# Kernel tuning notes

Hardware: AMD Instinct MI355X
Metric: run time of the kernel (lower is better)

The kernel has to match this reference:

```python
import jax, jax.numpy as jnp
import numpy as np

H = 1024
NH = 16
DH = H // NH

def setup_inputs() -> dict:
    key = jax.random.key(0)
    ks = jax.random.split(key, 6)
    s = 1.0 / np.sqrt(H)
    x = jax.random.normal(ks[0], (4, 2048, H), dtype=jnp.float32)
    Wq = jax.random.uniform(ks[1], (H, H), jnp.float32, -s, s)
    Wk = jax.random.uniform(ks[2], (H, H), jnp.float32, -s, s)
    Wv = jax.random.uniform(ks[3], (H, H), jnp.float32, -s, s)
    Wo = jax.random.uniform(ks[4], (H, H), jnp.float32, -s, s)
    bo = jax.random.uniform(ks[5], (H,), jnp.float32, -s, s)
    return {"x": x, "Wq": Wq, "Wk": Wk, "Wv": Wv, "Wo": Wo, "bo": bo}

def reference(x, Wq, Wk, Wv, Wo, bo):
    B, T, Hd = x.shape
    # projections: torch Linear is x @ W.T
    def split_heads(y):
        return y.reshape(B, T, NH, DH).transpose(0, 2, 1, 3)  # [B, nh, T, dh]
    Q = split_heads(x @ Wq.T)
    K = split_heads(x @ Wk.T)
    V = split_heads(x @ Wv.T)
    scores = jnp.einsum('bhtd,bhsd->bhts', Q, K) / jnp.sqrt(jnp.float32(DH))
    w = jax.nn.softmax(scores, axis=-1)
    ctx = jnp.einsum('bhts,bhsd->bhtd', w, V)  # [B, nh, T, dh]
    ctx = ctx.transpose(0, 2, 1, 3).reshape(B, T, Hd)
    out = ctx @ Wo.T + bo  # [B, T, H]
    return out.mean(axis=1)  # [B, H]
```

## Files before the change

kernel.cpp:

```cpp
#include <hip/hip_runtime.h>
#include <hip/hip_bf16.h>
#include <cstdint>

#define BB   4
#define TT   2048
#define HH   1024
#define NHH  16
#define DHH  64
#define MM   (BB*TT)
#define N3   (3*HH)

typedef __attribute__((ext_vector_type(8))) short short8;
typedef __attribute__((ext_vector_type(4))) float f32x4;

#if __has_builtin(__builtin_amdgcn_exp2f)
#define EXP2F(x) __builtin_amdgcn_exp2f(x)
#else
#define EXP2F(x) exp2f(x)
#endif

#define QSCALE 0.1803368801111204f

__device__ __forceinline__ float bf2f(unsigned short u) {
    return __uint_as_float(((uint32_t)u) << 16);
}
__device__ __forceinline__ unsigned short f2bf(float f) {
    uint32_t u = __float_as_uint(f);
    return (unsigned short)((u + 0x7fffu + ((u >> 16) & 1u)) >> 16);
}
__device__ __forceinline__ void gload_lds16(const unsigned short* g, unsigned short* l) {
    __builtin_amdgcn_global_load_lds(
        (const __attribute__((address_space(1))) uint32_t*)g,
        (__attribute__((address_space(3))) uint32_t*)l, 16, 0, 0);
}

__global__ __launch_bounds__(256) void cvt_bf16(
    const float* __restrict__ src, unsigned short* __restrict__ dst, int n4)
{
    int i = blockIdx.x * 256 + threadIdx.x;
    const int stride = gridDim.x * 256;
    for (; i < n4; i += stride) {
        float4 v = ((const float4*)src)[i];
        ushort4 o;
        o.x = f2bf(v.x); o.y = f2bf(v.y); o.z = f2bf(v.z); o.w = f2bf(v.w);
        ((ushort4*)dst)[i] = o;
    }
}

__global__ __launch_bounds__(256) void cvt_w3(
    const float* __restrict__ Wq, const float* __restrict__ Wk,
    const float* __restrict__ Wv, unsigned short* __restrict__ Wb)
{
    const float* src = (blockIdx.y == 0) ? Wq : (blockIdx.y == 1 ? Wk : Wv);
    unsigned short* dst = Wb + (size_t)blockIdx.y * HH * HH;
    const int n4 = HH * HH / 4;
    int i = blockIdx.x * 256 + threadIdx.x;
    const int stride = gridDim.x * 256;
    for (; i < n4; i += stride) {
        float4 v = ((const float4*)src)[i];
        ushort4 o;
        o.x = f2bf(v.x); o.y = f2bf(v.y); o.z = f2bf(v.z); o.w = f2bf(v.w);
        ((ushort4*)dst)[i] = o;
    }
}

__global__ __launch_bounds__(256) void proj_mfma(
    const unsigned short* __restrict__ xb, const unsigned short* __restrict__ Wb,
    unsigned short* __restrict__ qp, unsigned short* __restrict__ kp,
    unsigned short* __restrict__ vp)
{
    __shared__ unsigned short As[4096];
    __shared__ unsigned short Bs[4096];
    const int m0 = blockIdx.x * 128;
    const int n0 = blockIdx.y * 128;
    const int sel = n0 >> 10;
    const unsigned short* Wbase = Wb + (size_t)sel * HH * HH;
    const int nw0 = n0 & (HH - 1);
    const int tid = threadIdx.x;
    const int wave = tid >> 6, lane = tid & 63;
    const int quad = lane >> 4, l15 = lane & 15;
    const int wm = wave >> 1, wn = wave & 1;

    f32x4 acc[4][4];
    #pragma unroll
    for (int i = 0; i < 4; ++i)
        #pragma unroll
        for (int j = 0; j < 4; ++j) acc[i][j] = (f32x4){0.f, 0.f, 0.f, 0.f};

    for (int k0 = 0; k0 < HH; k0 += 32) {
        __syncthreads();
        #pragma unroll
        for (int q = 0; q < 2; ++q) {
            const int chunk = (wave * 2 + q) * 64 + lane;
            const int kc = chunk >> 7, mrow = chunk & 127;
            gload_lds16(xb    + (size_t)(m0  + mrow) * HH + k0 + kc * 8, As + chunk * 8);
            gload_lds16(Wbase + (size_t)(nw0 + mrow) * HH + k0 + kc * 8, Bs + chunk * 8);
        }
        __syncthreads();
        short8 af[4], bf[4];
        #pragma unroll
        for (int i = 0; i < 4; ++i)
            af[i] = *(const short8*)&As[(quad * 128 + wm * 64 + i * 16 + l15) * 8];
        #pragma unroll
        for (int j = 0; j < 4; ++j)
            bf[j] = *(const short8*)&Bs[(quad * 128 + wn * 64 + j * 16 + l15) * 8];
        #pragma unroll
        for (int i = 0; i < 4; ++i)
            #pragma unroll
            for (int j = 0; j < 4; ++j)
                acc[i][j] = __builtin_amdgcn_mfma_f32_16x16x32_bf16(af[i], bf[j], acc[i][j], 0, 0, 0);
    }

    unsigned short* outp = (sel == 0) ? qp : (sel == 1 ? kp : vp);
    const float cscale = (sel == 0) ? QSCALE : 1.0f;

    unsigned short* eb = As;
    const int lr_st = tid >> 3;
    const int k8    = tid & 7;
    const int row_g = m0 + ((lr_st & 16) ? 64 : 0) + (lr_st & 15);
    #pragma unroll
    for (int i = 0; i < 4; ++i) {
        __syncthreads();
        #pragma unroll
        for (int j = 0; j < 4; ++j) {
            const int c = wn * 64 + j * 16 + l15;
            #pragma unroll
            for (int r = 0; r < 4; ++r)
                eb[(wm * 16 + quad * 4 + r) * 128 + c] = f2bf(acc[i][j][r] * cscale);
        }
        __syncthreads();
        const int row = row_g + i * 16;
        const int bb2 = row >> 11, tt2 = row & (TT - 1);
        {
            const int col = n0 + k8 * 8;
            const int hh2 = (col >> 6) & (NHH - 1);
            *(short8*)(&outp[((size_t)(bb2 * NHH + hh2) * TT + tt2) * DHH + (col & 63)]) =
                *(const short8*)(&eb[lr_st * 128 + k8 * 8]);
        }
        {
            const int col = n0 + 64 + k8 * 8;
            const int hh2 = (col >> 6) & (NHH - 1);
            *(short8*)(&outp[((size_t)(bb2 * NHH + hh2) * TT + tt2) * DHH + (col & 63)]) =
                *(const short8*)(&eb[lr_st * 128 + 64 + k8 * 8]);
        }
    }
}

__global__ __launch_bounds__(256) void attn_fused(
    const unsigned short* __restrict__ qp, const unsigned short* __restrict__ kp,
    float* __restrict__ a)
{
    const int h = blockIdx.x, b = blockIdx.z;
    const int t0 = blockIdx.y * 128;
    const int bh = b * NHH + h;
    const int tid = threadIdx.x;
    const int wave = tid >> 6, lane = tid & 63;
    const int quad = lane >> 4, l15 = lane & 15;
    __shared__ float red[4][128];
    __shared__ float linv[128];

    const unsigned short* q = qp + (size_t)bh * TT * DHH;
    const unsigned short* kbase =
        kp + (size_t)bh * TT * DHH + (size_t)(wave * 512 + l15) * DHH + quad * 8;

    short8 aq[8][2];
    #pragma unroll
    for (int i = 0; i < 8; ++i)
        #pragma unroll
        for (int c = 0; c < 2; ++c)
            aq[i][c] = *(const short8*)&q[(size_t)(t0 + i * 16 + l15) * DHH + quad * 8 + c * 32];

    const f32x4 zk = {0.f, 0.f, 0.f, 0.f};

    float rs[8][4];
    #pragma unroll
    for (int i = 0; i < 8; ++i)
        #pragma unroll
        for (int r = 0; r < 4; ++r) rs[i][r] = 0.f;

    {
        const unsigned short* kw = kbase;
        short8 c0a = *(const short8*)(kw);
        short8 c0b = *(const short8*)(kw + 32);
        kw += 16 * DHH;
        short8 c1a = *(const short8*)(kw);
        short8 c1b = *(const short8*)(kw + 32);
        kw += 16 * DHH;
        for (int ss = 0; ss < 32; ++ss) {
            const short8 ba = c0a, bb = c0b;
            c0a = c1a; c0b = c1b;
            if (ss < 30) {
                c1a = *(const short8*)(kw);
                c1b = *(const short8*)(kw + 32);
            }
            kw += 16 * DHH;
            f32x4 pc = __builtin_amdgcn_mfma_f32_16x16x32_bf16(aq[0][0], ba, zk, 0, 0, 0);
            pc = __builtin_amdgcn_mfma_f32_16x16x32_bf16(aq[0][1], bb, pc, 0, 0, 0);
            #pragma unroll
            for (int i = 1; i < 8; ++i) {
                f32x4 c = __builtin_amdgcn_mfma_f32_16x16x32_bf16(aq[i][0], ba, zk, 0, 0, 0);
                c = __builtin_amdgcn_mfma_f32_16x16x32_bf16(aq[i][1], bb, c, 0, 0, 0);
                #pragma unroll
                for (int r = 0; r < 4; ++r) rs[i - 1][r] += EXP2F(pc[r]);
                pc = c;
            }
            #pragma unroll
            for (int r = 0; r < 4; ++r) rs[7][r] += EXP2F(pc[r]);
        }
    }
    #pragma unroll
    for (int off = 1; off < 16; off <<= 1)
        #pragma unroll
        for (int i = 0; i < 8; ++i)
            #pragma unroll
            for (int r = 0; r < 4; ++r) rs[i][r] += __shfl_xor(rs[i][r], off);
    if (l15 == 0)
        #pragma unroll
        for (int i = 0; i < 8; ++i)
            #pragma unroll
            for (int r = 0; r < 4; ++r) red[wave][i * 16 + quad * 4 + r] = rs[i][r];
    __syncthreads();
    if (tid < 128) {
        const float l = red[0][tid] + red[1][tid] + red[2][tid] + red[3][tid];
        linv[tid] = 1.0f / (l * (float)TT);
    }
    __syncthreads();

    float lrv[8][4];
    #pragma unroll
    for (int i = 0; i < 8; ++i)
        #pragma unroll
        for (int r = 0; r < 4; ++r) lrv[i][r] = linv[i * 16 + quad * 4 + r];

    float* ap = a + (size_t)bh * TT + wave * 512 + l15;

    {
        const unsigned short* kw = kbase;
        short8 c0a = *(const short8*)(kw);
        short8 c0b = *(const short8*)(kw + 32);
        kw += 16 * DHH;
        short8 c1a = *(const short8*)(kw);
        short8 c1b = *(const short8*)(kw + 32);
        kw += 16 * DHH;
        for (int ss = 0; ss < 32; ++ss) {
            const short8 ba = c0a, bb = c0b;
            c0a = c1a; c0b = c1b;
            if (ss < 30) {
                c1a = *(const short8*)(kw);
                c1b = *(const short8*)(kw + 32);
            }
            kw += 16 * DHH;
            float cs = 0.f;
            f32x4 pc = __builtin_amdgcn_mfma_f32_16x16x32_bf16(aq[0][0], ba, zk, 0, 0, 0);
            pc = __builtin_amdgcn_mfma_f32_16x16x32_bf16(aq[0][1], bb, pc, 0, 0, 0);
            #pragma unroll
            for (int i = 1; i < 8; ++i) {
                f32x4 c = __builtin_amdgcn_mfma_f32_16x16x32_bf16(aq[i][0], ba, zk, 0, 0, 0);
                c = __builtin_amdgcn_mfma_f32_16x16x32_bf16(aq[i][1], bb, c, 0, 0, 0);
                #pragma unroll
                for (int r = 0; r < 4; ++r) cs += EXP2F(pc[r]) * lrv[i - 1][r];
                pc = c;
            }
            #pragma unroll
            for (int r = 0; r < 4; ++r) cs += EXP2F(pc[r]) * lrv[7][r];
            cs += __shfl_xor(cs, 16);
            cs += __shfl_xor(cs, 32);
            if (lane < 16)
                atomicAdd(&ap[ss * 16], cs);
        }
    }
}

__global__ __launch_bounds__(256) void ctx_mean(
    const unsigned short* __restrict__ vp, const float* __restrict__ a,
    float* __restrict__ cm)
{
    const int h = blockIdx.x, b = blockIdx.y, sb = blockIdx.z;
    const int tid = threadIdx.x;
    const int d = tid & 63, sg = tid >> 6;
    const int bh = b * NHH + h;
    __shared__ float red[4][64];
    float part = 0.f;
    for (int s = sb * 256 + sg; s < sb * 256 + 256; s += 4) {
        const float av = a[(size_t)bh * TT + s];
        part += av * bf2f(vp[((size_t)bh * TT + s) * DHH + d]);
    }
    red[sg][d] = part;
    __syncthreads();
    if (tid < 64)
        atomicAdd(&cm[b * HH + h * DHH + tid],
                  red[0][tid] + red[1][tid] + red[2][tid] + red[3][tid]);
}

__global__ __launch_bounds__(256) void out_proj(
    const float* __restrict__ cm, const float* __restrict__ Wo,
    const float* __restrict__ bo, float* __restrict__ out)
{
    const int b = blockIdx.y;
    const int jb = blockIdx.x;
    const int tid = threadIdx.x;
    const int j = jb * 64 + (tid >> 2);
    const int kg = tid & 3;
    __shared__ float cs[HH];
    for (int k = tid; k < HH; k += 256) cs[k] = cm[b * HH + k];
    __syncthreads();
    float acc = 0.f;
    const float* wrow = &Wo[(size_t)j * HH];
    #pragma unroll 8
    for (int i = 0; i < 64; ++i) {
        const int k = kg * 256 + i * 4;
        float4 w4 = *(const float4*)&wrow[k];
        acc += w4.x * cs[k] + w4.y * cs[k+1] + w4.z * cs[k+2] + w4.w * cs[k+3];
    }
    acc += __shfl_down(acc, 2, 4);
    acc += __shfl_down(acc, 1, 4);
    if (kg == 0) out[b * HH + j] = acc + bo[j];
}

extern "C" void kernel_launch(void* const* d_in, const int* in_sizes, int n_in,
                              void* d_out, int out_size, void* d_ws, size_t ws_size,
                              hipStream_t stream) {
    const float* x  = (const float*)d_in[0];
    const float* Wq = (const float*)d_in[1];
    const float* Wk = (const float*)d_in[2];
    const float* Wv = (const float*)d_in[3];
    const float* Wo = (const float*)d_in[4];
    const float* bo = (const float*)d_in[5];
    float* out = (float*)d_out;

    char* ws = (char*)d_ws;
    unsigned short* qp = (unsigned short*)ws;  ws += (size_t)MM * HH * 2;
    unsigned short* kp = (unsigned short*)ws;  ws += (size_t)MM * HH * 2;
    unsigned short* vp = (unsigned short*)ws;  ws += (size_t)MM * HH * 2;
    unsigned short* xb = (unsigned short*)ws;  ws += (size_t)MM * HH * 2;
    unsigned short* Wb = (unsigned short*)ws;  ws += (size_t)3 * HH * HH * 2;
    float* a  = (float*)ws;                    ws += (size_t)BB * NHH * TT * 4;
    float* cm = (float*)ws;

    hipMemsetAsync(a, 0, (size_t)(BB * NHH * TT + BB * HH) * 4, stream);

    cvt_bf16<<<2048, 256, 0, stream>>>(x, xb, MM * HH / 4);
    cvt_w3  <<<dim3(512, 3), 256, 0, stream>>>(Wq, Wk, Wv, Wb);

    proj_mfma <<<dim3(64, 24),      256, 0, stream>>>(xb, Wb, qp, kp, vp);
    attn_fused<<<dim3(NHH, 16, BB), 256, 0, stream>>>(qp, kp, a);
    ctx_mean  <<<dim3(NHH, BB, 8),  256, 0, stream>>>(vp, a, cm);
    out_proj  <<<dim3(16, BB),      256, 0, stream>>>(cm, Wo, bo, out);
}
```

Before: 321.4 us.

## Replace two-pass attention with single-pass flash-style kernel using transposed V

The old two-pass attention, which recomputed QK^T to get row sums and then atomically accumulated column weights before a separate ctx_mean kernel, is replaced by a single-pass kernel. It computes exp scores once, stages them as bf16 in shared memory, and multiplies by a transposed V (written by the projection kernel) with MFMA, normalising per row at the end. This removes the second QK^T pass, the intermediate weight buffer, and a kernel launch. In exchange it adds P·V MFMA work and transposed V stores, and it uses no running max, relying on scores being small.

New measurement: 436.1 us. +35.7%, slower.

```diff
diff --git a/kernel.cpp b/kernel.cpp
--- a/kernel.cpp
+++ b/kernel.cpp
@@ -8,7 +8,6 @@
 #define NHH  16
 #define DHH  64
 #define MM   (BB*TT)
-#define N3   (3*HH)
 
 typedef __attribute__((ext_vector_type(8))) short short8;
 typedef __attribute__((ext_vector_type(4))) float f32x4;
@@ -27,6 +26,9 @@
 __device__ __forceinline__ unsigned short f2bf(float f) {
     uint32_t u = __float_as_uint(f);
     return (unsigned short)((u + 0x7fffu + ((u >> 16) & 1u)) >> 16);
+}
+__device__ __forceinline__ uint32_t pkbf(float lo, float hi) {
+    return (uint32_t)f2bf(lo) | ((uint32_t)f2bf(hi) << 16);
 }
 __device__ __forceinline__ void gload_lds16(const unsigned short* g, unsigned short* l) {
     __builtin_amdgcn_global_load_lds(
@@ -129,167 +131,157 @@
                 eb[(wm * 16 + quad * 4 + r) * 128 + c] = f2bf(acc[i][j][r] * cscale);
         }
         __syncthreads();
-        const int row = row_g + i * 16;
-        const int bb2 = row >> 11, tt2 = row & (TT - 1);
-        {
-            const int col = n0 + k8 * 8;
-            const int hh2 = (col >> 6) & (NHH - 1);
-            *(short8*)(&outp[((size_t)(bb2 * NHH + hh2) * TT + tt2) * DHH + (col & 63)]) =
-                *(const short8*)(&eb[lr_st * 128 + k8 * 8]);
-        }
-        {
-            const int col = n0 + 64 + k8 * 8;
-            const int hh2 = (col >> 6) & (NHH - 1);
-            *(short8*)(&outp[((size_t)(bb2 * NHH + hh2) * TT + tt2) * DHH + (col & 63)]) =
-                *(const short8*)(&eb[lr_st * 128 + 64 + k8 * 8]);
-        }
-    }
-}
-
-__global__ __launch_bounds__(256) void attn_fused(
+        if (sel < 2) {
+            const int row = row_g + i * 16;
+            const int bb2 = row >> 11, tt2 = row & (TT - 1);
+            {
+                const int col = n0 + k8 * 8;
+                const int hh2 = (col >> 6) & (NHH - 1);
+                *(short8*)(&outp[((size_t)(bb2 * NHH + hh2) * TT + tt2) * DHH + (col & 63)]) =
+                    *(const short8*)(&eb[lr_st * 128 + k8 * 8]);
+            }
+            {
+                const int col = n0 + 64 + k8 * 8;
+                const int hh2 = (col >> 6) & (NHH - 1);
+                *(short8*)(&outp[((size_t)(bb2 * NHH + hh2) * TT + tt2) * DHH + (col & 63)]) =
+                    *(const short8*)(&eb[lr_st * 128 + 64 + k8 * 8]);
+            }
+        } else {
+            const int c = tid & 127;
+            const int rn = tid >> 7;
+            const int colg = nw0 + c;
+            const int hh2 = (colg >> 6) & (NHH - 1);
+            const int dd = colg & 63;
+            #pragma unroll
+            for (int rr = 0; rr < 2; ++rr) {
+                const int run = rn + rr * 2;
+                const int tb = m0 + ((run >= 2) ? 64 : 0) + i * 16 + (run & 1) * 8;
+                const int bb2 = tb >> 11, tt2 = tb & (TT - 1);
+                short8 v;
+                #pragma unroll
+                for (int j = 0; j < 8; ++j)
+                    v[j] = (short)eb[(run * 8 + j) * 128 + c];
+                *(short8*)(&outp[((size_t)(bb2 * NHH + hh2) * DHH + dd) * TT + tt2]) = v;
+            }
+        }
+    }
+}
+
+__global__ __launch_bounds__(256) void attn_flash(
     const unsigned short* __restrict__ qp, const unsigned short* __restrict__ kp,
-    float* __restrict__ a)
+    const unsigned short* __restrict__ vt, float* __restrict__ cm)
 {
     const int h = blockIdx.x, b = blockIdx.z;
-    const int t0 = blockIdx.y * 128;
     const int bh = b * NHH + h;
     const int tid = threadIdx.x;
     const int wave = tid >> 6, lane = tid & 63;
     const int quad = lane >> 4, l15 = lane & 15;
-    __shared__ float red[4][128];
-    __shared__ float linv[128];
-
-    const unsigned short* q = qp + (size_t)bh * TT * DHH;
-    const unsigned short* kbase =
-        kp + (size_t)bh * TT * DHH + (size_t)(wave * 512 + l15) * DHH + quad * 8;
-
-    short8 aq[8][2];
-    #pragma unroll
-    for (int i = 0; i < 8; ++i)
+    const int t0w = blockIdx.y * 128 + wave * 32;
+
+    __shared__ unsigned short paT[4][2][16][40];
+
+    const unsigned short* q  = qp + (size_t)bh * TT * DHH;
+    const unsigned short* kb = kp + (size_t)bh * TT * DHH + l15 * DHH + quad * 8;
+    const unsigned short* vb = vt + ((size_t)bh * DHH + l15) * TT + quad * 8;
+
+    short8 aq[2][2];
+    #pragma unroll
+    for (int g = 0; g < 2; ++g)
         #pragma unroll
         for (int c = 0; c < 2; ++c)
-            aq[i][c] = *(const short8*)&q[(size_t)(t0 + i * 16 + l15) * DHH + quad * 8 + c * 32];
+            aq[g][c] = *(const short8*)&q[(size_t)(t0w + g * 16 + l15) * DHH + quad * 8 + c * 32];
 
     const f32x4 zk = {0.f, 0.f, 0.f, 0.f};
-
-    float rs[8][4];
-    #pragma unroll
-    for (int i = 0; i < 8; ++i)
-        #pragma unroll
-        for (int r = 0; r < 4; ++r) rs[i][r] = 0.f;
-
-    {
-        const unsigned short* kw = kbase;
-        short8 c0a = *(const short8*)(kw);
-        short8 c0b = *(const short8*)(kw + 32);
-        kw += 16 * DHH;
-        short8 c1a = *(const short8*)(kw);
-        short8 c1b = *(const short8*)(kw + 32);
-        kw += 16 * DHH;
-        for (int ss = 0; ss < 32; ++ss) {
-            const short8 ba = c0a, bb = c0b;
-            c0a = c1a; c0b = c1b;
-            if (ss < 30) {
-                c1a = *(const short8*)(kw);
-                c1b = *(const short8*)(kw + 32);
-            }
-            kw += 16 * DHH;
-            f32x4 pc = __builtin_amdgcn_mfma_f32_16x16x32_bf16(aq[0][0], ba, zk, 0, 0, 0);
-            pc = __builtin_amdgcn_mfma_f32_16x16x32_bf16(aq[0][1], bb, pc, 0, 0, 0);
-            #pragma unroll
-            for (int i = 1; i < 8; ++i) {
-                f32x4 c = __builtin_amdgcn_mfma_f32_16x16x32_bf16(aq[i][0], ba, zk, 0, 0, 0);
-                c = __builtin_amdgcn_mfma_f32_16x16x32_bf16(aq[i][1], bb, c, 0, 0, 0);
-                #pragma unroll
-                for (int r = 0; r < 4; ++r) rs[i - 1][r] += EXP2F(pc[r]);
-                pc = c;
-            }
-            #pragma unroll
-            for (int r = 0; r < 4; ++r) rs[7][r] += EXP2F(pc[r]);
-        }
-    }
-    #pragma unroll
-    for (int off = 1; off < 16; off <<= 1)
-        #pragma unroll
-        for (int i = 0; i < 8; ++i)
-            #pragma unroll
-            for (int r = 0; r < 4; ++r) rs[i][r] += __shfl_xor(rs[i][r], off);
-    if (l15 == 0)
-        #pragma unroll
-        for (int i = 0; i < 8; ++i)
-            #pragma unroll
-            for (int r = 0; r < 4; ++r) red[wave][i * 16 + quad * 4 + r] = rs[i][r];
-    __syncthreads();
-    if (tid < 128) {
-        const float l = red[0][tid] + red[1][tid] + red[2][tid] + red[3][tid];
-        linv[tid] = 1.0f / (l * (float)TT);
-    }
-    __syncthreads();
-
-    float lrv[8][4];
-    #pragma unroll
-    for (int i = 0; i < 8; ++i)
-        #pragma unroll
-        for (int r = 0; r < 4; ++r) lrv[i][r] = linv[i * 16 + quad * 4 + r];
-
-    float* ap = a + (size_t)bh * TT + wave * 512 + l15;
-
-    {
-        const unsigned short* kw = kbase;
-        short8 c0a = *(const short8*)(kw);
-        short8 c0b = *(const short8*)(kw + 32);
-        kw += 16 * DHH;
-        short8 c1a = *(const short8*)(kw);
-        short8 c1b = *(const short8*)(kw + 32);
-        kw += 16 * DHH;
-        for (int ss = 0; ss < 32; ++ss) {
-            const short8 ba = c0a, bb = c0b;
-            c0a = c1a; c0b = c1b;
-            if (ss < 30) {
-                c1a = *(const short8*)(kw);
-                c1b = *(const short8*)(kw + 32);
-            }
-            kw += 16 * DHH;
-            float cs = 0.f;
-            f32x4 pc = __builtin_amdgcn_mfma_f32_16x16x32_bf16(aq[0][0], ba, zk, 0, 0, 0);
-            pc = __builtin_amdgcn_mfma_f32_16x16x32_bf16(aq[0][1], bb, pc, 0, 0, 0);
-            #pragma unroll
-            for (int i = 1; i < 8; ++i) {
-                f32x4 c = __builtin_amdgcn_mfma_f32_16x16x32_bf16(aq[i][0], ba, zk, 0, 0, 0);
-                c = __builtin_amdgcn_mfma_f32_16x16x32_bf16(aq[i][1], bb, c, 0, 0, 0);
-                #pragma unroll
-                for (int r = 0; r < 4; ++r) cs += EXP2F(pc[r]) * lrv[i - 1][r];
-                pc = c;
-            }
-            #pragma unroll
-            for (int r = 0; r < 4; ++r) cs += EXP2F(pc[r]) * lrv[7][r];
-            cs += __shfl_xor(cs, 16);
-            cs += __shfl_xor(cs, 32);
-            if (lane < 16)
-                atomicAdd(&ap[ss * 16], cs);
-        }
-    }
-}
-
-__global__ __launch_bounds__(256) void ctx_mean(
-    const unsigned short* __restrict__ vp, const float* __restrict__ a,
-    float* __restrict__ cm)
-{
-    const int h = blockIdx.x, b = blockIdx.y, sb = blockIdx.z;
-    const int tid = threadIdx.x;
-    const int d = tid & 63, sg = tid >> 6;
-    const int bh = b * NHH + h;
-    __shared__ float red[4][64];
-    float part = 0.f;
-    for (int s = sb * 256 + sg; s < sb * 256 + 256; s += 4) {
-        const float av = a[(size_t)bh * TT + s];
-        part += av * bf2f(vp[((size_t)bh * TT + s) * DHH + d]);
-    }
-    red[sg][d] = part;
-    __syncthreads();
-    if (tid < 64)
-        atomicAdd(&cm[b * HH + h * DHH + tid],
-                  red[0][tid] + red[1][tid] + red[2][tid] + red[3][tid]);
+    f32x4 acc[2][4];
+    #pragma unroll
+    for (int g = 0; g < 2; ++g)
+        #pragma unroll
+        for (int dc = 0; dc < 4; ++dc) acc[g][dc] = zk;
+    float den0 = 0.f, den1 = 0.f;
+
+    short8 kf00 = *(const short8*)(kb);
+    short8 kf01 = *(const short8*)(kb + 32);
+    short8 kf10 = *(const short8*)(kb + 16 * DHH);
+    short8 kf11 = *(const short8*)(kb + 16 * DHH + 32);
+
+    for (int ss = 0; ss < 64; ++ss) {
+        const int so = ss * 32;
+        short8 vf0 = *(const short8*)(vb + (size_t)0 * 16 * TT + so);
+        short8 vf1 = *(const short8*)(vb + (size_t)1 * 16 * TT + so);
+        short8 vf2 = *(const short8*)(vb + (size_t)2 * 16 * TT + so);
+        short8 vf3 = *(const short8*)(vb + (size_t)3 * 16 * TT + so);
+
+        f32x4 s00 = __builtin_amdgcn_mfma_f32_16x16x32_bf16(kf00, aq[0][0], zk, 0, 0, 0);
+        s00 = __builtin_amdgcn_mfma_f32_16x16x32_bf16(kf01, aq[0][1], s00, 0, 0, 0);
+        f32x4 s01 = __builtin_amdgcn_mfma_f32_16x16x32_bf16(kf10, aq[0][0], zk, 0, 0, 0);
+        s01 = __builtin_amdgcn_mfma_f32_16x16x32_bf16(kf11, aq[0][1], s01, 0, 0, 0);
+        f32x4 s10 = __builtin_amdgcn_mfma_f32_16x16x32_bf16(kf00, aq[1][0], zk, 0, 0, 0);
+        s10 = __builtin_amdgcn_mfma_f32_16x16x32_bf16(kf01, aq[1][1], s10, 0, 0, 0);
+        f32x4 s11 = __builtin_amdgcn_mfma_f32_16x16x32_bf16(kf10, aq[1][0], zk, 0, 0, 0);
+        s11 = __builtin_amdgcn_mfma_f32_16x16x32_bf16(kf11, aq[1][1], s11, 0, 0, 0);
+
+        if (ss < 63) {
+            const unsigned short* kn = kb + (size_t)(so + 32) * DHH;
+            kf00 = *(const short8*)(kn);
+            kf01 = *(const short8*)(kn + 32);
+            kf10 = *(const short8*)(kn + 16 * DHH);
+            kf11 = *(const short8*)(kn + 16 * DHH + 32);
+        }
+
+        {
+            float e0 = EXP2F(s00[0]), e1 = EXP2F(s00[1]), e2 = EXP2F(s00[2]), e3 = EXP2F(s00[3]);
+            den0 += (e0 + e1) + (e2 + e3);
+            *(uint32_t*)&paT[wave][0][l15][4 * quad]      = pkbf(e0, e1);
+            *(uint32_t*)&paT[wave][0][l15][4 * quad + 2]  = pkbf(e2, e3);
+        }
+        {
+            float e0 = EXP2F(s01[0]), e1 = EXP2F(s01[1]), e2 = EXP2F(s01[2]), e3 = EXP2F(s01[3]);
+            den0 += (e0 + e1) + (e2 + e3);
+            *(uint32_t*)&paT[wave][0][l15][16 + 4 * quad]     = pkbf(e0, e1);
+            *(uint32_t*)&paT[wave][0][l15][16 + 4 * quad + 2] = pkbf(e2, e3);
+        }
+        {
+            float e0 = EXP2F(s10[0]), e1 = EXP2F(s10[1]), e2 = EXP2F(s10[2]), e3 = EXP2F(s10[3]);
+            den1 += (e0 + e1) + (e2 + e3);
+            *(uint32_t*)&paT[wave][1][l15][4 * quad]      = pkbf(e0, e1);
+            *(uint32_t*)&paT[wave][1][l15][4 * quad + 2]  = pkbf(e2, e3);
+        }
+        {
+            float e0 = EXP2F(s11[0]), e1 = EXP2F(s11[1]), e2 = EXP2F(s11[2]), e3 = EXP2F(s11[3]);
+            den1 += (e0 + e1) + (e2 + e3);
+            *(uint32_t*)&paT[wave][1][l15][16 + 4 * quad]     = pkbf(e0, e1);
+            *(uint32_t*)&paT[wave][1][l15][16 + 4 * quad + 2] = pkbf(e2, e3);
+        }
+
+        short8 pa0 = *(const short8*)&paT[wave][0][l15][quad * 8];
+        short8 pa1 = *(const short8*)&paT[wave][1][l15][quad * 8];
+
+        acc[0][0] = __builtin_amdgcn_mfma_f32_16x16x32_bf16(vf0, pa0, acc[0][0], 0, 0, 0);
+        acc[0][1] = __builtin_amdgcn_mfma_f32_16x16x32_bf16(vf1, pa0, acc[0][1], 0, 0, 0);
+        acc[0][2] = __builtin_amdgcn_mfma_f32_16x16x32_bf16(vf2, pa0, acc[0][2], 0, 0, 0);
+        acc[0][3] = __builtin_amdgcn_mfma_f32_16x16x32_bf16(vf3, pa0, acc[0][3], 0, 0, 0);
+        acc[1][0] = __builtin_amdgcn_mfma_f32_16x16x32_bf16(vf0, pa1, acc[1][0], 0, 0, 0);
+        acc[1][1] = __builtin_amdgcn_mfma_f32_16x16x32_bf16(vf1, pa1, acc[1][1], 0, 0, 0);
+        acc[1][2] = __builtin_amdgcn_mfma_f32_16x16x32_bf16(vf2, pa1, acc[1][2], 0, 0, 0);
+        acc[1][3] = __builtin_amdgcn_mfma_f32_16x16x32_bf16(vf3, pa1, acc[1][3], 0, 0, 0);
+    }
+
+    den0 += __shfl_xor(den0, 16); den0 += __shfl_xor(den0, 32);
+    den1 += __shfl_xor(den1, 16); den1 += __shfl_xor(den1, 32);
+    const float inv0 = 1.0f / (den0 * (float)TT);
+    const float inv1 = 1.0f / (den1 * (float)TT);
+
+    #pragma unroll
+    for (int dc = 0; dc < 4; ++dc) {
+        #pragma unroll
+        for (int r = 0; r < 4; ++r) {
+            float v = acc[0][dc][r] * inv0 + acc[1][dc][r] * inv1;
+            v += __shfl_xor(v, 1); v += __shfl_xor(v, 2);
+            v += __shfl_xor(v, 4); v += __shfl_xor(v, 8);
+            if (l15 == 0)
+                atomicAdd(&cm[b * HH + h * DHH + dc * 16 + quad * 4 + r], v);
+        }
+    }
 }
 
 __global__ __launch_bounds__(256) void out_proj(
@@ -331,19 +323,17 @@
     char* ws = (char*)d_ws;
     unsigned short* qp = (unsigned short*)ws;  ws += (size_t)MM * HH * 2;
     unsigned short* kp = (unsigned short*)ws;  ws += (size_t)MM * HH * 2;
-    unsigned short* vp = (unsigned short*)ws;  ws += (size_t)MM * HH * 2;
+    unsigned short* vt = (unsigned short*)ws;  ws += (size_t)MM * HH * 2;
     unsigned short* xb = (unsigned short*)ws;  ws += (size_t)MM * HH * 2;
     unsigned short* Wb = (unsigned short*)ws;  ws += (size_t)3 * HH * HH * 2;
-    float* a  = (float*)ws;                    ws += (size_t)BB * NHH * TT * 4;
     float* cm = (float*)ws;
 
-    hipMemsetAsync(a, 0, (size_t)(BB * NHH * TT + BB * HH) * 4, stream);
+    hipMemsetAsync(cm, 0, (size_t)BB * HH * 4, stream);
 
     cvt_bf16<<<2048, 256, 0, stream>>>(x, xb, MM * HH / 4);
     cvt_w3  <<<dim3(512, 3), 256, 0, stream>>>(Wq, Wk, Wv, Wb);
 
-    proj_mfma <<<dim3(64, 24),      256, 0, stream>>>(xb, Wb, qp, kp, vp);
-    attn_fused<<<dim3(NHH, 16, BB), 256, 0, stream>>>(qp, kp, a);
-    ctx_mean  <<<dim3(NHH, BB, 8),  256, 0, stream>>>(vp, a, cm);
+    proj_mfma <<<dim3(64, 24),      256, 0, stream>>>(xb, Wb, qp, kp, vt);
+    attn_flash<<<dim3(NHH, 16, BB), 256, 0, stream>>>(qp, kp, vt, cm);
     out_proj  <<<dim3(16, BB),      256, 0, stream>>>(cm, Wo, bo, out);
 }
```
